# Kernel optimization log

Hardware: AMD Instinct MI355X
Metric: run time of the kernel (lower is better)

Reference implementation:

```python
import jax, jax.numpy as jnp
import numpy as np

B, S, D_MODEL, D_INNER = 64, 128, 1024, 1024


def setup_inputs() -> dict:
    key = jax.random.key(0)
    ks = jax.random.split(key, 10)
    sc = 0.02
    return {
        "embeddings": jax.random.normal(ks[0], (B, S, D_MODEL), dtype=jnp.float32),
        "Wq": jax.random.normal(ks[1], (D_MODEL, D_INNER), dtype=jnp.float32) * sc,
        "bq": jnp.zeros((D_INNER,), dtype=jnp.float32),
        "Wk": jax.random.normal(ks[2], (D_MODEL, D_INNER), dtype=jnp.float32) * sc,
        "bk": jnp.zeros((D_INNER,), dtype=jnp.float32),
        "Wv": jax.random.normal(ks[3], (D_MODEL, D_INNER), dtype=jnp.float32) * sc,
        "bv": jnp.zeros((D_INNER,), dtype=jnp.float32),
        "w": jax.random.normal(ks[4], (S, S), dtype=jnp.float32) * sc,
        "Wo": jax.random.normal(ks[5], (D_INNER, D_MODEL), dtype=jnp.float32) * sc,
        "bo": jnp.zeros((D_MODEL,), dtype=jnp.float32),
    }


def reference(embeddings, Wq, bq, Wk, bk, Wv, bv, w, Wo, bo):
    # embeddings: [B, S, Dm]
    seq_len = embeddings.shape[1]
    q = embeddings @ Wq + bq          # [B, S, Di]
    k = embeddings @ Wk + bk
    v = embeddings @ Wv + bv

    max_k = jnp.max(k, axis=1, keepdims=True)   # [B, 1, Di]
    exp_k = jnp.exp(k - max_k)                  # [B, S, Di]

    max_w = jnp.max(w, axis=1, keepdims=True)   # [S, 1]
    wn = w - max_w                              # [S, S]
    tril = jnp.tril(jnp.ones((seq_len, seq_len), dtype=bool))
    wn = jnp.where(tril, wn[:seq_len, :seq_len], -jnp.inf)
    # torch.einsum('bjj,bjd->bjd', exp_w, x) picks the DIAGONAL of exp_w
    # (repeated subscript j) and multiplies elementwise along the seq dim.
    diag_w = jnp.exp(jnp.diagonal(wn))          # [S]; tril diagonal is True so finite
    dw = diag_w[None, :, None]                  # [1, S, 1]

    numerator = dw * (exp_k * v)                # [B, S, Di]
    denominator = dw * exp_k                    # [B, S, Di]
    out = jax.nn.sigmoid(q) * (numerator / denominator)
    return out @ Wo + bo                        # [B, S, Dm]
```

## Files before the change

### kernel.cpp

```cpp
#include <hip/hip_runtime.h>


typedef short bf16x8 __attribute__((ext_vector_type(8)));
typedef float f32x4  __attribute__((ext_vector_type(4)));

__device__ __forceinline__ short f2bf(float f) {
  union { float f; unsigned u; } x; x.f = f;
  unsigned r = x.u + 0x7fffu + ((x.u >> 16) & 1u);
  return (short)(r >> 16);
}

struct alignas(16) S8 { short v[8]; };

#define GLDS(g, l) \
  __builtin_amdgcn_global_load_lds((const __attribute__((address_space(1))) void*)(g), \
                                   (__attribute__((address_space(3))) void*)(l), 16, 0, 0)
#define BAR()    __builtin_amdgcn_s_barrier()
#define PRIO(x)  __builtin_amdgcn_s_setprio(x)
#define SCHED0() __builtin_amdgcn_sched_barrier(0)
#define VMCNT(N) asm volatile("s_waitcnt vmcnt(" #N ")" ::: "memory")
#define LGKM0()  asm volatile("s_waitcnt lgkmcnt(0)" ::: "memory")
#define MFMA(a, b, c) __builtin_amdgcn_mfma_f32_16x16x32_bf16((a), (b), (c), 0, 0, 0)

__global__ __launch_bounds__(256) void prep_kernel(
    const float* __restrict__ emb, const float* __restrict__ Wq, const float* __restrict__ Wv,
    const float* __restrict__ Wo, short* __restrict__ embB, short* __restrict__ WqvT,
    short* __restrict__ WoT) {
  __shared__ float tr[64 * 65];
  const int t = threadIdx.x;
  const int bid = blockIdx.x;
  const int gdim = gridDim.x;

  for (size_t i = (size_t)bid * 256 + t; i < 1048576; i += (size_t)gdim * 256) {
    const float4* p = (const float4*)emb + i * 2;
    float4 a = p[0], b = p[1];
    S8 s;
    s.v[0] = f2bf(a.x); s.v[1] = f2bf(a.y); s.v[2] = f2bf(a.z); s.v[3] = f2bf(a.w);
    s.v[4] = f2bf(b.x); s.v[5] = f2bf(b.y); s.v[6] = f2bf(b.z); s.v[7] = f2bf(b.w);
    ((S8*)embB)[i] = s;
  }

  const int rr = t >> 4, cc4 = (t & 15) * 4;
  const int orow = t >> 3, ocol8 = (t & 7) * 8;
  for (int z = bid; z < 768; z += gdim) {
    const float* in; short* op; int ti;
    if (z < 256)      { in = Wq; op = WqvT;           ti = z; }
    else if (z < 512) { in = Wv; op = WqvT + 1048576; ti = z - 256; }
    else              { in = Wo; op = WoT;            ti = z - 512; }
    const int bx = (ti & 15) * 64, by = (ti >> 4) * 64;
    __syncthreads();
#pragma unroll
    for (int k = 0; k < 4; ++k) {
      float4 v = *(const float4*)&in[(size_t)(by + rr + 16 * k) * 1024 + bx + cc4];
      float* d = &tr[(rr + 16 * k) * 65 + cc4];
      d[0] = v.x; d[1] = v.y; d[2] = v.z; d[3] = v.w;
    }
    __syncthreads();
#pragma unroll
    for (int h = 0; h < 2; ++h) {
      const int oc = orow + 32 * h;
      S8 s;
#pragma unroll
      for (int i = 0; i < 8; ++i) s.v[i] = f2bf(tr[(ocol8 + i) * 65 + oc]);
      *(S8*)&op[(size_t)(bx + oc) * 1024 + by + ocol8] = s;
    }
  }
}

__global__ __launch_bounds__(512, 2) void gemm_qv_kernel(
    const short* __restrict__ A, const short* __restrict__ BT,
    const float* __restrict__ bq, const float* __restrict__ bv, short* __restrict__ X) {
  __shared__ short As[2][256 * 64];
  __shared__ short Bqs[2][128 * 64];
  __shared__ short Bvs[2][128 * 64];
  const int t = threadIdx.x;
  const int lane = t & 63;
  const int w = t >> 6;
  const int l16 = lane & 15;
  const int quad = lane >> 4;
  const int b = blockIdx.x;
  const int wg = (b & 7) * 32 + (b >> 3);
  const int bm = (wg >> 3) * 256;
  const int bn = (wg & 7) * 128;
  const int wm = (w & 3) * 64;
  const int wn = (w >> 2) * 64;

  const int r8 = t >> 3;
  const int swe = ((t & 7) ^ (r8 & 7)) * 8;
  const short* gA = A + (size_t)(bm + r8) * 1024 + swe;
  const short* gq = BT + (size_t)(bn + r8) * 1024 + swe;
  const short* gv = BT + (size_t)(1024 + bn + r8) * 1024 + swe;
  short* lA = &As[0][0] + w * 512;
  short* lq = &Bqs[0][0] + w * 512;
  short* lv = &Bvs[0][0] + w * 512;

#define QV_STAGE(k, s) do {                                             \
    const short* a_ = gA + (k) * 64; short* la_ = lA + (s) * 16384;     \
    GLDS(a_, la_);               GLDS(a_ + 64 * 1024, la_ + 4096);      \
    GLDS(a_ + 128 * 1024, la_ + 8192); GLDS(a_ + 192 * 1024, la_ + 12288); \
    const short* q_ = gq + (k) * 64; short* lq_ = lq + (s) * 8192;      \
    GLDS(q_, lq_);               GLDS(q_ + 64 * 1024, lq_ + 4096);      \
    const short* v_ = gv + (k) * 64; short* lv_ = lv + (s) * 8192;      \
    GLDS(v_, lv_);               GLDS(v_ + 64 * 1024, lv_ + 4096);      \
  } while (0)

  const int csw0 = (quad ^ (l16 & 7)) * 8;
  const int csw1 = ((quad + 4) ^ (l16 & 7)) * 8;
  const short* fA0 = &As[0][0] + (wm + l16) * 64 + csw0;
  const short* fA1 = &As[0][0] + (wm + l16) * 64 + csw1;
  const short* fq0 = &Bqs[0][0] + (wn + l16) * 64 + csw0;
  const short* fq1 = &Bqs[0][0] + (wn + l16) * 64 + csw1;
  const short* fv0 = &Bvs[0][0] + (wn + l16) * 64 + csw0;
  const short* fv1 = &Bvs[0][0] + (wn + l16) * 64 + csw1;

  f32x4 aq[4][4] = {};
  f32x4 av[4][4] = {};

  QV_STAGE(0, 0);
  QV_STAGE(1, 1);

  for (int j = 0; j < 16; ++j) {
    const int s = j & 1;
    const short* sA0 = fA0 + s * 16384;
    const short* sA1 = fA1 + s * 16384;
    const short* sq0 = fq0 + s * 8192;
    const short* sq1 = fq1 + s * 8192;
    const short* sv0 = fv0 + s * 8192;
    const short* sv1 = fv1 + s * 8192;

    if (j < 15) { VMCNT(8); } else { VMCNT(0); }
    BAR();

    bf16x8 a0[4], a1[4], bq0[4], bq1[4], bv0[4], bv1[4];
#pragma unroll
    for (int i = 0; i < 4; ++i) {
      a0[i] = *(const bf16x8*)(sA0 + i * 1024);
      a1[i] = *(const bf16x8*)(sA1 + i * 1024);
      bq0[i] = *(const bf16x8*)(sq0 + i * 1024);
    }
    BAR(); LGKM0(); SCHED0(); PRIO(1);
#pragma unroll
    for (int i = 0; i < 4; ++i)
#pragma unroll
      for (int n = 0; n < 4; ++n)
        aq[i][n] = MFMA(a0[i], bq0[n], aq[i][n]);
    PRIO(0); BAR();
#pragma unroll
    for (int i = 0; i < 4; ++i) {
      bq1[i] = *(const bf16x8*)(sq1 + i * 1024);
      bv0[i] = *(const bf16x8*)(sv0 + i * 1024);
      bv1[i] = *(const bf16x8*)(sv1 + i * 1024);
    }
    BAR(); LGKM0(); SCHED0(); PRIO(1);
#pragma unroll
    for (int i = 0; i < 4; ++i)
#pragma unroll
      for (int n = 0; n < 4; ++n)
        aq[i][n] = MFMA(a1[i], bq1[n], aq[i][n]);
    PRIO(0); BAR();
    if (j < 14) {
      const short* a_ = gA + (j + 2) * 64; short* la_ = lA + s * 16384;
      GLDS(a_, la_);                     GLDS(a_ + 64 * 1024, la_ + 4096);
      GLDS(a_ + 128 * 1024, la_ + 8192); GLDS(a_ + 192 * 1024, la_ + 12288);
    }
    PRIO(1);
#pragma unroll
    for (int i = 0; i < 4; ++i)
#pragma unroll
      for (int n = 0; n < 4; ++n)
        av[i][n] = MFMA(a0[i], bv0[n], av[i][n]);
    PRIO(0); BAR();
    if (j < 14) {
      const short* q_ = gq + (j + 2) * 64; short* lq_ = lq + s * 8192;
      GLDS(q_, lq_); GLDS(q_ + 64 * 1024, lq_ + 4096);
      const short* v_ = gv + (j + 2) * 64; short* lv_ = lv + s * 8192;
      GLDS(v_, lv_); GLDS(v_ + 64 * 1024, lv_ + 4096);
    }
    PRIO(1);
#pragma unroll
    for (int i = 0; i < 4; ++i)
#pragma unroll
      for (int n = 0; n < 4; ++n)
        av[i][n] = MFMA(a1[i], bv1[n], av[i][n]);
    PRIO(0); BAR();
  }
#undef QV_STAGE

#pragma unroll
  for (int n = 0; n < 4; ++n) {
    const int col = bn + wn + n * 16 + l16;
    const float bql = bq[col], bvl = bv[col];
#pragma unroll
    for (int i = 0; i < 4; ++i)
#pragma unroll
      for (int r = 0; r < 4; ++r) {
        const int row = bm + wm + i * 16 + quad * 4 + r;
        const float q = aq[i][n][r] + bql;
        const float v = av[i][n][r] + bvl;
        const float sg = 1.0f / (1.0f + __expf(-q));
        X[(size_t)row * 1024 + col] = f2bf(sg * v);
      }
  }
}

__global__ __launch_bounds__(512, 2) void gemm_bt_kernel(
    const short* __restrict__ A, const short* __restrict__ BT, float* __restrict__ C,
    const float* __restrict__ bias) {
  __shared__ short As[2][256 * 64];
  __shared__ short Bs[2][128 * 64];
  const int t = threadIdx.x;
  const int lane = t & 63;
  const int w = t >> 6;
  const int l16 = lane & 15;
  const int quad = lane >> 4;
  const int b = blockIdx.x;
  const int wg = (b & 7) * 32 + (b >> 3);
  const int bm = (wg >> 3) * 256;
  const int bn = (wg & 7) * 128;
  const int wm = (w & 3) * 64;
  const int wn = (w >> 2) * 64;

  const int r8 = t >> 3;
  const int swe = ((t & 7) ^ (r8 & 7)) * 8;
  const short* gA = A + (size_t)(bm + r8) * 1024 + swe;
  const short* gB = BT + (size_t)(bn + r8) * 1024 + swe;
  short* lA = &As[0][0] + w * 512;
  short* lB = &Bs[0][0] + w * 512;

#define BT_STAGE(k, s) do {                                             \
    const short* a_ = gA + (k) * 64; short* la_ = lA + (s) * 16384;     \
    GLDS(a_, la_);               GLDS(a_ + 64 * 1024, la_ + 4096);      \
    GLDS(a_ + 128 * 1024, la_ + 8192); GLDS(a_ + 192 * 1024, la_ + 12288); \
    const short* b_ = gB + (k) * 64; short* lb_ = lB + (s) * 8192;      \
    GLDS(b_, lb_);               GLDS(b_ + 64 * 1024, lb_ + 4096);      \
  } while (0)

  const int csw0 = (quad ^ (l16 & 7)) * 8;
  const int csw1 = ((quad + 4) ^ (l16 & 7)) * 8;
  const short* fA0 = &As[0][0] + (wm + l16) * 64 + csw0;
  const short* fA1 = &As[0][0] + (wm + l16) * 64 + csw1;
  const short* fB0 = &Bs[0][0] + (wn + l16) * 64 + csw0;
  const short* fB1 = &Bs[0][0] + (wn + l16) * 64 + csw1;

  f32x4 acc[4][4] = {};

  BT_STAGE(0, 0);
  BT_STAGE(1, 1);

  for (int j = 0; j < 16; ++j) {
    const int s = j & 1;
    const short* sA0 = fA0 + s * 16384;
    const short* sA1 = fA1 + s * 16384;
    const short* sB0 = fB0 + s * 8192;
    const short* sB1 = fB1 + s * 8192;

    if (j < 15) { VMCNT(6); } else { VMCNT(0); }
    BAR();

    bf16x8 a0[4], a1[4], b0[4], b1[4];
#pragma unroll
    for (int i = 0; i < 4; ++i) {
      a0[i] = *(const bf16x8*)(sA0 + i * 1024);
      a1[i] = *(const bf16x8*)(sA1 + i * 1024);
      b0[i] = *(const bf16x8*)(sB0 + i * 1024);
    }
    BAR(); LGKM0(); SCHED0(); PRIO(1);
#pragma unroll
    for (int i = 0; i < 4; ++i)
#pragma unroll
      for (int n = 0; n < 2; ++n)
        acc[i][n] = MFMA(a0[i], b0[n], acc[i][n]);
    PRIO(0); BAR();
#pragma unroll
    for (int i = 0; i < 4; ++i) b1[i] = *(const bf16x8*)(sB1 + i * 1024);
    BAR(); LGKM0(); SCHED0(); PRIO(1);
#pragma unroll
    for (int i = 0; i < 4; ++i)
#pragma unroll
      for (int n = 0; n < 2; ++n)
        acc[i][2 + n] = MFMA(a0[i], b0[2 + n], acc[i][2 + n]);
    PRIO(0); BAR();
    if (j < 14) {
      const short* a_ = gA + (j + 2) * 64; short* la_ = lA + s * 16384;
      GLDS(a_, la_); GLDS(a_ + 64 * 1024, la_ + 4096);
      GLDS(a_ + 128 * 1024, la_ + 8192);
    }
    PRIO(1);
#pragma unroll
    for (int i = 0; i < 4; ++i)
#pragma unroll
      for (int n = 0; n < 2; ++n)
        acc[i][n] = MFMA(a1[i], b1[n], acc[i][n]);
    PRIO(0); BAR();
    if (j < 14) {
      const short* a_ = gA + (j + 2) * 64; short* la_ = lA + s * 16384;
      GLDS(a_ + 192 * 1024, la_ + 12288);
      const short* b_ = gB + (j + 2) * 64; short* lb_ = lB + s * 8192;
      GLDS(b_, lb_); GLDS(b_ + 64 * 1024, lb_ + 4096);
    }
    PRIO(1);
#pragma unroll
    for (int i = 0; i < 4; ++i)
#pragma unroll
      for (int n = 0; n < 2; ++n)
        acc[i][2 + n] = MFMA(a1[i], b1[2 + n], acc[i][2 + n]);
    PRIO(0); BAR();
  }
#undef BT_STAGE

#pragma unroll
  for (int n = 0; n < 4; ++n) {
    const int col = bn + wn + n * 16 + l16;
    const float bl = bias[col];
#pragma unroll
    for (int i = 0; i < 4; ++i)
#pragma unroll
      for (int r = 0; r < 4; ++r) {
        const int row = bm + wm + i * 16 + quad * 4 + r;
        C[(size_t)row * 1024 + col] = acc[i][n][r] + bl;
      }
  }
}

extern "C" void kernel_launch(void* const* d_in, const int* in_sizes, int n_in,
                              void* d_out, int out_size, void* d_ws, size_t ws_size,
                              hipStream_t stream) {
  const float* emb = (const float*)d_in[0];
  const float* Wq  = (const float*)d_in[1];
  const float* bq  = (const float*)d_in[2];
  const float* Wv  = (const float*)d_in[5];
  const float* bv  = (const float*)d_in[6];
  const float* Wo  = (const float*)d_in[8];
  const float* bo  = (const float*)d_in[9];
  float* out = (float*)d_out;

  char* ws = (char*)d_ws;
  short* embB = (short*)(ws);
  short* X    = (short*)(ws + 16777216);
  short* WqvT = (short*)(ws + 33554432);
  short* WoT  = (short*)(ws + 37748736);

  prep_kernel<<<256, 256, 0, stream>>>(emb, Wq, Wv, Wo, embB, WqvT, WoT);
  gemm_qv_kernel<<<256, 512, 0, stream>>>(embB, WqvT, bq, bv, X);
  gemm_bt_kernel<<<256, 512, 0, stream>>>(X, WoT, out, bo);
}
```

Measured before the change: 167.7 us.

## Simplify output GEMM to single-buffered 128x128 tiles and enlarge prep grid

Replaces the double-buffered 256x128 output-projection GEMM, which had interleaved prefetch and priority scheduling, with a plain single-buffered 128x128 tile kernel. It launches 512 blocks of 256 threads, with a load, barrier, compute, barrier pattern on each K step. The prep kernel's launch grid grows from 256 to 768 blocks. The simpler kernel aims to raise occupancy and block count, but it gives up the overlap of global loads with MFMA work.

```diff
diff --git a/kernel.cpp b/kernel.cpp
--- a/kernel.cpp
+++ b/kernel.cpp
@@ -203,121 +203,78 @@
   }
 }
 
-__global__ __launch_bounds__(512, 2) void gemm_bt_kernel(
+__global__ __launch_bounds__(256) void gemm_bt_kernel(
     const short* __restrict__ A, const short* __restrict__ BT, float* __restrict__ C,
     const float* __restrict__ bias) {
-  __shared__ short As[2][256 * 64];
-  __shared__ short Bs[2][128 * 64];
+  __shared__ short As[128 * 64];
+  __shared__ short Bs[128 * 64];
   const int t = threadIdx.x;
   const int lane = t & 63;
   const int w = t >> 6;
   const int l16 = lane & 15;
   const int quad = lane >> 4;
-  const int b = blockIdx.x;
-  const int wg = (b & 7) * 32 + (b >> 3);
-  const int bm = (wg >> 3) * 256;
-  const int bn = (wg & 7) * 128;
-  const int wm = (w & 3) * 64;
-  const int wn = (w >> 2) * 64;
+  const int bm = blockIdx.x * 128;
+  const int bn = blockIdx.y * 128;
+  const int wm = (w & 1) * 64;
+  const int wn = (w >> 1) * 64;
 
   const int r8 = t >> 3;
   const int swe = ((t & 7) ^ (r8 & 7)) * 8;
-  const short* gA = A + (size_t)(bm + r8) * 1024 + swe;
-  const short* gB = BT + (size_t)(bn + r8) * 1024 + swe;
-  short* lA = &As[0][0] + w * 512;
-  short* lB = &Bs[0][0] + w * 512;
-
-#define BT_STAGE(k, s) do {                                             \
-    const short* a_ = gA + (k) * 64; short* la_ = lA + (s) * 16384;     \
-    GLDS(a_, la_);               GLDS(a_ + 64 * 1024, la_ + 4096);      \
-    GLDS(a_ + 128 * 1024, la_ + 8192); GLDS(a_ + 192 * 1024, la_ + 12288); \
-    const short* b_ = gB + (k) * 64; short* lb_ = lB + (s) * 8192;      \
-    GLDS(b_, lb_);               GLDS(b_ + 64 * 1024, lb_ + 4096);      \
-  } while (0)
-
-  const int csw0 = (quad ^ (l16 & 7)) * 8;
-  const int csw1 = ((quad + 4) ^ (l16 & 7)) * 8;
-  const short* fA0 = &As[0][0] + (wm + l16) * 64 + csw0;
-  const short* fA1 = &As[0][0] + (wm + l16) * 64 + csw1;
-  const short* fB0 = &Bs[0][0] + (wn + l16) * 64 + csw0;
-  const short* fB1 = &Bs[0][0] + (wn + l16) * 64 + csw1;
+  const short* pA0 = A + (size_t)(bm + r8) * 1024 + swe;
+  const short* pA1 = pA0 + 32 * 1024;
+  const short* pA2 = pA0 + 64 * 1024;
+  const short* pA3 = pA0 + 96 * 1024;
+  const short* pB0 = BT + (size_t)(bn + r8) * 1024 + swe;
+  const short* pB1 = pB0 + 32 * 1024;
+  const short* pB2 = pB0 + 64 * 1024;
+  const short* pB3 = pB0 + 96 * 1024;
+  short* lA = As + w * 512;
+  short* lB = Bs + w * 512;
+
+  const int qsw0 = (quad ^ (l16 & 7)) * 8;
+  const int qsw1 = ((quad + 4) ^ (l16 & 7)) * 8;
+  const short* fA0 = As + (wm + l16) * 64 + qsw0;
+  const short* fA1 = As + (wm + l16) * 64 + qsw1;
+  const short* fB0 = Bs + (wn + l16) * 64 + qsw0;
+  const short* fB1 = Bs + (wn + l16) * 64 + qsw1;
 
   f32x4 acc[4][4] = {};
 
-  BT_STAGE(0, 0);
-  BT_STAGE(1, 1);
-
-  for (int j = 0; j < 16; ++j) {
-    const int s = j & 1;
-    const short* sA0 = fA0 + s * 16384;
-    const short* sA1 = fA1 + s * 16384;
-    const short* sB0 = fB0 + s * 8192;
-    const short* sB1 = fB1 + s * 8192;
-
-    if (j < 15) { VMCNT(6); } else { VMCNT(0); }
-    BAR();
-
-    bf16x8 a0[4], a1[4], b0[4], b1[4];
-#pragma unroll
-    for (int i = 0; i < 4; ++i) {
-      a0[i] = *(const bf16x8*)(sA0 + i * 1024);
-      a1[i] = *(const bf16x8*)(sA1 + i * 1024);
-      b0[i] = *(const bf16x8*)(sB0 + i * 1024);
-    }
-    BAR(); LGKM0(); SCHED0(); PRIO(1);
-#pragma unroll
-    for (int i = 0; i < 4; ++i)
-#pragma unroll
-      for (int n = 0; n < 2; ++n)
-        acc[i][n] = MFMA(a0[i], b0[n], acc[i][n]);
-    PRIO(0); BAR();
-#pragma unroll
-    for (int i = 0; i < 4; ++i) b1[i] = *(const bf16x8*)(sB1 + i * 1024);
-    BAR(); LGKM0(); SCHED0(); PRIO(1);
-#pragma unroll
-    for (int i = 0; i < 4; ++i)
-#pragma unroll
-      for (int n = 0; n < 2; ++n)
-        acc[i][2 + n] = MFMA(a0[i], b0[2 + n], acc[i][2 + n]);
-    PRIO(0); BAR();
-    if (j < 14) {
-      const short* a_ = gA + (j + 2) * 64; short* la_ = lA + s * 16384;
-      GLDS(a_, la_); GLDS(a_ + 64 * 1024, la_ + 4096);
-      GLDS(a_ + 128 * 1024, la_ + 8192);
-    }
-    PRIO(1);
-#pragma unroll
-    for (int i = 0; i < 4; ++i)
-#pragma unroll
-      for (int n = 0; n < 2; ++n)
-        acc[i][n] = MFMA(a1[i], b1[n], acc[i][n]);
-    PRIO(0); BAR();
-    if (j < 14) {
-      const short* a_ = gA + (j + 2) * 64; short* la_ = lA + s * 16384;
-      GLDS(a_ + 192 * 1024, la_ + 12288);
-      const short* b_ = gB + (j + 2) * 64; short* lb_ = lB + s * 8192;
-      GLDS(b_, lb_); GLDS(b_ + 64 * 1024, lb_ + 4096);
-    }
-    PRIO(1);
-#pragma unroll
-    for (int i = 0; i < 4; ++i)
-#pragma unroll
-      for (int n = 0; n < 2; ++n)
-        acc[i][2 + n] = MFMA(a1[i], b1[2 + n], acc[i][2 + n]);
-    PRIO(0); BAR();
-  }
-#undef BT_STAGE
-
-#pragma unroll
-  for (int n = 0; n < 4; ++n) {
-    const int col = bn + wn + n * 16 + l16;
-    const float bl = bias[col];
-#pragma unroll
-    for (int i = 0; i < 4; ++i)
-#pragma unroll
-      for (int r = 0; r < 4; ++r) {
-        const int row = bm + wm + i * 16 + quad * 4 + r;
-        C[(size_t)row * 1024 + col] = acc[i][n][r] + bl;
+  for (int it = 0; it < 16; ++it) {
+    GLDS(pA0, lA); GLDS(pA1, lA + 2048); GLDS(pA2, lA + 4096); GLDS(pA3, lA + 6144);
+    GLDS(pB0, lB); GLDS(pB1, lB + 2048); GLDS(pB2, lB + 4096); GLDS(pB3, lB + 6144);
+    pA0 += 64; pA1 += 64; pA2 += 64; pA3 += 64;
+    pB0 += 64; pB1 += 64; pB2 += 64; pB3 += 64;
+    __syncthreads();
+
+#pragma unroll
+    for (int h = 0; h < 2; h++) {
+      const short* fA = h ? fA1 : fA0;
+      const short* fB = h ? fB1 : fB0;
+      bf16x8 av[4], bw[4];
+#pragma unroll
+      for (int i = 0; i < 4; i++) av[i] = *(const bf16x8*)(fA + i * 1024);
+#pragma unroll
+      for (int j = 0; j < 4; j++) bw[j] = *(const bf16x8*)(fB + j * 1024);
+#pragma unroll
+      for (int i = 0; i < 4; i++)
+#pragma unroll
+        for (int j = 0; j < 4; j++)
+          acc[i][j] = MFMA(av[i], bw[j], acc[i][j]);
+    }
+    __syncthreads();
+  }
+
+#pragma unroll
+  for (int j = 0; j < 4; j++) {
+    int col = bn + wn + j * 16 + l16;
+    float bl = bias[col];
+#pragma unroll
+    for (int i = 0; i < 4; i++)
+#pragma unroll
+      for (int r = 0; r < 4; r++) {
+        int row = bm + wm + i * 16 + quad * 4 + r;
+        C[(size_t)row * 1024 + col] = acc[i][j][r] + bl;
       }
   }
 }
@@ -340,7 +297,7 @@
   short* WqvT = (short*)(ws + 33554432);
   short* WoT  = (short*)(ws + 37748736);
 
-  prep_kernel<<<256, 256, 0, stream>>>(emb, Wq, Wv, Wo, embB, WqvT, WoT);
+  prep_kernel<<<768, 256, 0, stream>>>(emb, Wq, Wv, Wo, embB, WqvT, WoT);
   gemm_qv_kernel<<<256, 512, 0, stream>>>(embB, WqvT, bq, bv, X);
-  gemm_bt_kernel<<<256, 512, 0, stream>>>(X, WoT, out, bo);
-}
+  gemm_bt_kernel<<<dim3(64, 8), 256, 0, stream>>>(X, WoT, out, bo);
+}
```

After: 162.8 us, median of 2. 2.9% less time.

## Shrink output GEMM tile to 128x128, reorder LDS loads, enlarge prep grid

Applied to the files above, without the earlier changes.

The output projection GEMM moves from 256x128 tiles with 512 threads to 128x128 tiles with 256 threads on a 64x8 grid. This doubles the workgroup count so more work can be spread across compute units, and the staging and MFMA phases are restructured to match. The QV GEMM now splits its LDS fragment loads into three smaller phases so the loads for V overlap with the prefetch. The prep kernel launch grows from 256 to 768 blocks. Risks: smaller tiles give less operand reuse per block, the tile swizzle is dropped, and the prep kernel's indexing must actually handle the larger grid.

```diff
diff --git a/kernel.cpp b/kernel.cpp
--- a/kernel.cpp
+++ b/kernel.cpp
@@ -135,21 +135,19 @@
 #pragma unroll
     for (int i = 0; i < 4; ++i) {
       a0[i] = *(const bf16x8*)(sA0 + i * 1024);
+      bq0[i] = *(const bf16x8*)(sq0 + i * 1024);
+    }
+    BAR(); LGKM0(); SCHED0(); PRIO(1);
+#pragma unroll
+    for (int i = 0; i < 4; ++i)
+#pragma unroll
+      for (int n = 0; n < 4; ++n)
+        aq[i][n] = MFMA(a0[i], bq0[n], aq[i][n]);
+    PRIO(0); BAR();
+#pragma unroll
+    for (int i = 0; i < 4; ++i) {
       a1[i] = *(const bf16x8*)(sA1 + i * 1024);
-      bq0[i] = *(const bf16x8*)(sq0 + i * 1024);
-    }
-    BAR(); LGKM0(); SCHED0(); PRIO(1);
-#pragma unroll
-    for (int i = 0; i < 4; ++i)
-#pragma unroll
-      for (int n = 0; n < 4; ++n)
-        aq[i][n] = MFMA(a0[i], bq0[n], aq[i][n]);
-    PRIO(0); BAR();
-#pragma unroll
-    for (int i = 0; i < 4; ++i) {
       bq1[i] = *(const bf16x8*)(sq1 + i * 1024);
-      bv0[i] = *(const bf16x8*)(sv0 + i * 1024);
-      bv1[i] = *(const bf16x8*)(sv1 + i * 1024);
     }
     BAR(); LGKM0(); SCHED0(); PRIO(1);
 #pragma unroll
@@ -163,7 +161,12 @@
       GLDS(a_, la_);                     GLDS(a_ + 64 * 1024, la_ + 4096);
       GLDS(a_ + 128 * 1024, la_ + 8192); GLDS(a_ + 192 * 1024, la_ + 12288);
     }
-    PRIO(1);
+#pragma unroll
+    for (int i = 0; i < 4; ++i) {
+      bv0[i] = *(const bf16x8*)(sv0 + i * 1024);
+      bv1[i] = *(const bf16x8*)(sv1 + i * 1024);
+    }
+    BAR(); LGKM0(); SCHED0(); PRIO(1);
 #pragma unroll
     for (int i = 0; i < 4; ++i)
 #pragma unroll
@@ -203,22 +206,20 @@
   }
 }
 
-__global__ __launch_bounds__(512, 2) void gemm_bt_kernel(
+__global__ __launch_bounds__(256) void gemm_bt_kernel(
     const short* __restrict__ A, const short* __restrict__ BT, float* __restrict__ C,
     const float* __restrict__ bias) {
-  __shared__ short As[2][256 * 64];
+  __shared__ short As[2][128 * 64];
   __shared__ short Bs[2][128 * 64];
   const int t = threadIdx.x;
   const int lane = t & 63;
   const int w = t >> 6;
   const int l16 = lane & 15;
   const int quad = lane >> 4;
-  const int b = blockIdx.x;
-  const int wg = (b & 7) * 32 + (b >> 3);
-  const int bm = (wg >> 3) * 256;
-  const int bn = (wg & 7) * 128;
-  const int wm = (w & 3) * 64;
-  const int wn = (w >> 2) * 64;
+  const int bm = blockIdx.x * 128;
+  const int bn = blockIdx.y * 128;
+  const int wm = (w & 1) * 64;
+  const int wn = (w >> 1) * 64;
 
   const int r8 = t >> 3;
   const int swe = ((t & 7) ^ (r8 & 7)) * 8;
@@ -227,20 +228,21 @@
   short* lA = &As[0][0] + w * 512;
   short* lB = &Bs[0][0] + w * 512;
 
-#define BT_STAGE(k, s) do {                                             \
-    const short* a_ = gA + (k) * 64; short* la_ = lA + (s) * 16384;     \
-    GLDS(a_, la_);               GLDS(a_ + 64 * 1024, la_ + 4096);      \
-    GLDS(a_ + 128 * 1024, la_ + 8192); GLDS(a_ + 192 * 1024, la_ + 12288); \
-    const short* b_ = gB + (k) * 64; short* lb_ = lB + (s) * 8192;      \
-    GLDS(b_, lb_);               GLDS(b_ + 64 * 1024, lb_ + 4096);      \
+#define BT_STAGE(k, s) do {                                               \
+    const short* a_ = gA + (k) * 64; short* la_ = lA + (s) * 8192;        \
+    GLDS(a_, la_);                    GLDS(a_ + 32 * 1024, la_ + 2048);   \
+    GLDS(a_ + 64 * 1024, la_ + 4096); GLDS(a_ + 96 * 1024, la_ + 6144);   \
+    const short* b_ = gB + (k) * 64; short* lb_ = lB + (s) * 8192;        \
+    GLDS(b_, lb_);                    GLDS(b_ + 32 * 1024, lb_ + 2048);   \
+    GLDS(b_ + 64 * 1024, lb_ + 4096); GLDS(b_ + 96 * 1024, lb_ + 6144);   \
   } while (0)
 
-  const int csw0 = (quad ^ (l16 & 7)) * 8;
-  const int csw1 = ((quad + 4) ^ (l16 & 7)) * 8;
-  const short* fA0 = &As[0][0] + (wm + l16) * 64 + csw0;
-  const short* fA1 = &As[0][0] + (wm + l16) * 64 + csw1;
-  const short* fB0 = &Bs[0][0] + (wn + l16) * 64 + csw0;
-  const short* fB1 = &Bs[0][0] + (wn + l16) * 64 + csw1;
+  const int qsw0 = (quad ^ (l16 & 7)) * 8;
+  const int qsw1 = ((quad + 4) ^ (l16 & 7)) * 8;
+  const short* fA0 = &As[0][0] + (wm + l16) * 64 + qsw0;
+  const short* fA1 = &As[0][0] + (wm + l16) * 64 + qsw1;
+  const short* fB0 = &Bs[0][0] + (wn + l16) * 64 + qsw0;
+  const short* fB1 = &Bs[0][0] + (wn + l16) * 64 + qsw1;
 
   f32x4 acc[4][4] = {};
 
@@ -249,55 +251,40 @@
 
   for (int j = 0; j < 16; ++j) {
     const int s = j & 1;
-    const short* sA0 = fA0 + s * 16384;
-    const short* sA1 = fA1 + s * 16384;
+    const short* sA0 = fA0 + s * 8192;
+    const short* sA1 = fA1 + s * 8192;
     const short* sB0 = fB0 + s * 8192;
     const short* sB1 = fB1 + s * 8192;
 
-    if (j < 15) { VMCNT(6); } else { VMCNT(0); }
+    if (j < 15) { VMCNT(8); } else { VMCNT(0); }
     BAR();
 
     bf16x8 a0[4], a1[4], b0[4], b1[4];
 #pragma unroll
     for (int i = 0; i < 4; ++i) {
       a0[i] = *(const bf16x8*)(sA0 + i * 1024);
+      b0[i] = *(const bf16x8*)(sB0 + i * 1024);
+    }
+    BAR(); LGKM0(); SCHED0(); PRIO(1);
+#pragma unroll
+    for (int i = 0; i < 4; ++i)
+#pragma unroll
+      for (int n = 0; n < 4; ++n)
+        acc[i][n] = MFMA(a0[i], b0[n], acc[i][n]);
+    PRIO(0); BAR();
+#pragma unroll
+    for (int i = 0; i < 4; ++i) {
       a1[i] = *(const bf16x8*)(sA1 + i * 1024);
-      b0[i] = *(const bf16x8*)(sB0 + i * 1024);
-    }
-    BAR(); LGKM0(); SCHED0(); PRIO(1);
-#pragma unroll
-    for (int i = 0; i < 4; ++i)
-#pragma unroll
-      for (int n = 0; n < 2; ++n)
-        acc[i][n] = MFMA(a0[i], b0[n], acc[i][n]);
-    PRIO(0); BAR();
-#pragma unroll
-    for (int i = 0; i < 4; ++i) b1[i] = *(const bf16x8*)(sB1 + i * 1024);
-    BAR(); LGKM0(); SCHED0(); PRIO(1);
-#pragma unroll
-    for (int i = 0; i < 4; ++i)
-#pragma unroll
-      for (int n = 0; n < 2; ++n)
-        acc[i][2 + n] = MFMA(a0[i], b0[2 + n], acc[i][2 + n]);
-    PRIO(0); BAR();
-    if (j < 14) {
-      const short* a_ = gA + (j + 2) * 64; short* la_ = lA + s * 16384;
-      GLDS(a_, la_); GLDS(a_ + 64 * 1024, la_ + 4096);
-      GLDS(a_ + 128 * 1024, la_ + 8192);
-    }
-    PRIO(1);
+      b1[i] = *(const bf16x8*)(sB1 + i * 1024);
+    }
+    BAR(); LGKM0(); SCHED0(); PRIO(1);
 #pragma unroll
     for (int i = 0; i < 4; ++i)
 #pragma unroll
       for (int n = 0; n < 2; ++n)
         acc[i][n] = MFMA(a1[i], b1[n], acc[i][n]);
     PRIO(0); BAR();
-    if (j < 14) {
-      const short* a_ = gA + (j + 2) * 64; short* la_ = lA + s * 16384;
-      GLDS(a_ + 192 * 1024, la_ + 12288);
-      const short* b_ = gB + (j + 2) * 64; short* lb_ = lB + s * 8192;
-      GLDS(b_, lb_); GLDS(b_ + 64 * 1024, lb_ + 4096);
-    }
+    if (j < 14) BT_STAGE(j + 2, s);
     PRIO(1);
 #pragma unroll
     for (int i = 0; i < 4; ++i)
@@ -340,7 +327,7 @@
   short* WqvT = (short*)(ws + 33554432);
   short* WoT  = (short*)(ws + 37748736);
 
-  prep_kernel<<<256, 256, 0, stream>>>(emb, Wq, Wv, Wo, embB, WqvT, WoT);
+  prep_kernel<<<768, 256, 0, stream>>>(emb, Wq, Wv, Wo, embB, WqvT, WoT);
   gemm_qv_kernel<<<256, 512, 0, stream>>>(embB, WqvT, bq, bv, X);
-  gemm_bt_kernel<<<256, 512, 0, stream>>>(X, WoT, out, bo);
-}
+  gemm_bt_kernel<<<dim3(64, 8), 256, 0, stream>>>(X, WoT, out, bo);
+}
```

Result: no change. 164.9 us (-1.7%).
